# Kernel optimization log

Measured on AMD Instinct MI355X. Metric: run time of the kernel, lower is better.

## Reference

```python
import jax, jax.numpy as jnp
import numpy as np

E_LAYERS, D_MODEL, D_STATE, D_CONV, DT_RANK, D_FF = 2, 512, 16, 2, 32, 2048
BATCH, SEQ = 16, 512


def layer_norm(x, w, b, eps=1e-5):
    m = x.mean(-1, keepdims=True)
    v = ((x - m) ** 2).mean(-1, keepdims=True)
    return (x - m) / jnp.sqrt(v + eps) * w + b


def mamba(x, in_w, conv_w, conv_b, xproj_w, dt_w, dt_b, A_log, D_skip, out_w):
    # x: [B, L, D]; expand=1 so d_inner == D
    Bsz, L, D = x.shape
    N = A_log.shape[-1]
    R = dt_w.shape[-1]
    xz = x @ in_w.T                      # [B, L, 2D]
    xi, z = jnp.split(xz, 2, axis=-1)
    # causal depthwise conv1d, kernel K
    K = conv_w.shape[-1]
    xp = jnp.pad(xi.transpose(0, 2, 1), ((0, 0), (0, 0), (K - 1, 0)))  # [B, D, L+K-1]
    xc = jax.lax.conv_general_dilated(
        xp, conv_w[:, None, :], (1,), 'VALID',
        dimension_numbers=('NCH', 'OIH', 'NCH'), feature_group_count=D)  # [B, D, L]
    xc = jax.nn.silu(xc.transpose(0, 2, 1) + conv_b)                     # [B, L, D]
    proj = xc @ xproj_w.T                                                # [B, L, R+2N]
    dt, Bm, Cm = jnp.split(proj, [R, R + N], axis=-1)
    dt = jax.nn.softplus(dt @ dt_w.T + dt_b)                             # [B, L, D]
    A = -jnp.exp(A_log)                                                  # [D, N]
    dA = jnp.exp(dt[..., None] * A)                                      # [B, L, D, N]
    dBu = dt[..., None] * Bm[:, :, None, :] * xc[..., None]              # [B, L, D, N]

    def step(h, inp):
        a, b = inp
        h = a * h + b
        return h, h

    _, hs = jax.lax.scan(step, jnp.zeros((Bsz, D, N), x.dtype),
                         (dA.transpose(1, 0, 2, 3), dBu.transpose(1, 0, 2, 3)))
    y = jnp.einsum('lbdn,bln->bld', hs, Cm) + D_skip * xc
    return (y * jax.nn.silu(z)) @ out_w.T


def reference(x, in_w, conv_w, conv_b, xproj_w, dt_w, dt_b, A_log, D_skip, out_w,
              ffn1_w, ffn1_b, ffn2_w, ffn2_b, n1_w, n1_b, n2_w, n2_b, fn_w, fn_b):
    E = in_w.shape[0]
    for e in range(E):
        fwd = mamba(x, in_w[e, 0], conv_w[e, 0], conv_b[e, 0], xproj_w[e, 0],
                    dt_w[e, 0], dt_b[e, 0], A_log[e, 0], D_skip[e, 0], out_w[e, 0])
        xr = jnp.flip(x, axis=1)
        rev = mamba(xr, in_w[e, 1], conv_w[e, 1], conv_b[e, 1], xproj_w[e, 1],
                    dt_w[e, 1], dt_b[e, 1], A_log[e, 1], D_skip[e, 1], out_w[e, 1])
        x = x + fwd + jnp.flip(rev, axis=1)
        x = layer_norm(x, n1_w[e], n1_b[e])
        y = jax.nn.gelu(x @ ffn1_w[e].T + ffn1_b[e], approximate=False)
        y = y @ ffn2_w[e].T + ffn2_b[e]
        x = layer_norm(x + y, n2_w[e], n2_b[e])
    return layer_norm(x, fn_w, fn_b)


def setup_inputs() -> dict:
    key = jax.random.key(0)
    E, D, N, K, R, F = E_LAYERS, D_MODEL, D_STATE, D_CONV, DT_RANK, D_FF
    B, L = BATCH, SEQ
    ks = jax.random.split(key, 12)

    def rn(k, shape, s=0.02):
        return jax.random.normal(k, shape, jnp.float32) * s

    A_log = jnp.tile(jnp.log(jnp.arange(1, N + 1, dtype=jnp.float32)), (E, 2, D, 1))
    return {
        'x': jax.random.normal(ks[0], (B, L, D), jnp.float32),
        'in_w': rn(ks[1], (E, 2, 2 * D, D)),
        'conv_w': rn(ks[2], (E, 2, D, K), 0.5),
        'conv_b': jnp.zeros((E, 2, D), jnp.float32),
        'xproj_w': rn(ks[3], (E, 2, R + 2 * N, D)),
        'dt_w': rn(ks[4], (E, 2, D, R), 0.1),
        'dt_b': rn(ks[5], (E, 2, D), 0.1),
        'A_log': A_log,
        'D_skip': jnp.ones((E, 2, D), jnp.float32),
        'out_w': rn(ks[6], (E, 2, D, D)),
        'ffn1_w': rn(ks[7], (E, F, D)),
        'ffn1_b': jnp.zeros((E, F), jnp.float32),
        'ffn2_w': rn(ks[8], (E, D, F)),
        'ffn2_b': jnp.zeros((E, D), jnp.float32),
        'n1_w': jnp.ones((E, D), jnp.float32),
        'n1_b': jnp.zeros((E, D), jnp.float32),
        'n2_w': jnp.ones((E, D), jnp.float32),
        'n2_b': jnp.zeros((E, D), jnp.float32),
        'fn_w': jnp.ones((D,), jnp.float32),
        'fn_b': jnp.zeros((D,), jnp.float32),
    }
```

## Files before the change

### kernel.cpp

```cpp
#include <hip/hip_runtime.h>

#define BB 16
#define LL 512
#define DD 512
#define ROWS (BB*LL)

typedef unsigned short u16;
typedef __attribute__((ext_vector_type(8))) short short8;
typedef __attribute__((ext_vector_type(4))) float f32x4;
typedef __attribute__((ext_vector_type(4))) unsigned short u16x4;

__device__ __forceinline__ float b2f(u16 u) {
    return __uint_as_float(((unsigned int)u) << 16);
}
__device__ __forceinline__ u16 f2b(float f) {
    unsigned int u = __float_as_uint(f);
    u += 0x7FFFu + ((u >> 16) & 1u);
    return (u16)(u >> 16);
}
__device__ __forceinline__ float ld1(const void* p, size_t i, int f32) {
    return f32 ? ((const float*)p)[i] : b2f(((const u16*)p)[i]);
}
__device__ __forceinline__ float bf_elem(uint4 v, int j) {
    unsigned w = ((const unsigned*)&v)[j >> 1];
    return __uint_as_float((j & 1) ? (w & 0xFFFF0000u) : (w << 16));
}
__device__ __forceinline__ float red16(float x) {
    int v = __float_as_int(x);
    x += __int_as_float(__builtin_amdgcn_update_dpp(0, v, 0xB1, 0xF, 0xF, true));
    v = __float_as_int(x);
    x += __int_as_float(__builtin_amdgcn_update_dpp(0, v, 0x4E, 0xF, 0xF, true));
    v = __float_as_int(x);
    x += __int_as_float(__builtin_amdgcn_update_dpp(0, v, 0x141, 0xF, 0xF, true));
    v = __float_as_int(x);
    x += __int_as_float(__builtin_amdgcn_update_dpp(0, v, 0x140, 0xF, 0xF, true));
    return x;
}
__device__ __forceinline__ void gld16(const u16* g, u16* l) {
    __builtin_amdgcn_global_load_lds(
        (const __attribute__((address_space(1))) unsigned int*)g,
        (__attribute__((address_space(3))) unsigned int*)l, 16, 0, 0);
}

__global__ void detect(const u16* __restrict__ x, int* __restrict__ flag)
{
    __shared__ int s;
    if (threadIdx.x == 0) s = 0;
    __syncthreads();
    u16 v = x[2 * threadIdx.x] & 0x7FFFu;
    if ((v & 0x7F80u) >= 0x5000u) atomicOr(&s, 1);
    __syncthreads();
    if (threadIdx.x == 0) *flag = s;
}

__global__ __launch_bounds__(256)
void cvt_x(const void* __restrict__ X, float* __restrict__ acc, u16* __restrict__ cur,
           const int* __restrict__ flag)
{
    const int f = *flag;
    size_t i = (size_t)blockIdx.x * 256 + threadIdx.x;
    float v = ld1(X, i, f);
    acc[i] = v;
    cur[i] = f2b(v);
}

__global__ __launch_bounds__(256)
void cvt_copy(const void* __restrict__ src, u16* __restrict__ dst, int n,
              const int* __restrict__ flag)
{
    const int f = *flag;
    int i = blockIdx.x * 256 + threadIdx.x;
    if (i < n) dst[i] = f2b(ld1(src, i, f));
}

__global__ __launch_bounds__(256)
void cvt_xp2(const void* __restrict__ xp, u16* __restrict__ dst,
             const int* __restrict__ flag)
{
    const int f = *flag;
    int i = blockIdx.x * 256 + threadIdx.x;
    int e = i >> 17, r = (i >> 10) & 127, c = i & 1023;
    int dir = r >> 6, n = r & 63;
    float v = ((c >> 9) == dir)
        ? ld1(xp, ((size_t)(e*2 + dir)*64 + n)*512 + (c & 511), f) : 0.f;
    dst[i] = f2b(v);
}

__global__ __launch_bounds__(256)
void cvt_dt2(const void* __restrict__ dw, u16* __restrict__ dst,
             const int* __restrict__ flag)
{
    const int f = *flag;
    int i = blockIdx.x * 256 + threadIdx.x;
    int e = i >> 17, r = (i >> 7) & 1023, c = i & 127;
    int dir = r >> 9, d = r & 511;
    float v = 0.f;
    if (dir == 0 && c < 32)
        v = ld1(dw, ((size_t)(e*2)*512 + d)*32 + c, f);
    else if (dir == 1 && c >= 64 && c < 96)
        v = ld1(dw, ((size_t)(e*2 + 1)*512 + d)*32 + (c - 64), f);
    dst[i] = f2b(v);
}

__global__ __launch_bounds__(256)
void cvt_out2(const void* __restrict__ ow, u16* __restrict__ dst,
              const int* __restrict__ flag)
{
    const int f = *flag;
    int i = blockIdx.x * 256 + threadIdx.x;
    int e = i >> 19, rest = i & 524287;
    int d = rest >> 10, c = rest & 1023;
    int dir = c >> 9;
    dst[i] = f2b(ld1(ow, ((size_t)(e*2 + dir)*512 + d)*512 + (c & 511), f));
}

__global__ __launch_bounds__(256)
void acc_init(const u16* __restrict__ x, float* __restrict__ o)
{
    size_t i = (size_t)blockIdx.x * 256 + threadIdx.x;
    o[i] = b2f(x[i]);
}

__global__ __launch_bounds__(256)
void gemm_mfma(const u16* __restrict__ A, const u16* __restrict__ W,
               float* __restrict__ Cf, u16* __restrict__ Cb, u16* __restrict__ CbT,
               int M, int N, int K,
               const void* __restrict__ bias, size_t boff, int act, int accum,
               const int* __restrict__ flag)
{
    const int f = *flag;
    __shared__ u16 As[128][64];
    __shared__ u16 Ws[128][64];
    const int tid  = threadIdx.x;
    const int lane = tid & 63;
    const int wid  = tid >> 6;
    const int wr   = (wid >> 1) * 64;
    const int wc   = (wid & 1) * 64;
    const int row0 = blockIdx.y * 128;
    const int col0 = blockIdx.x * 128;
    const int mrow = lane & 15;
    const int kq   = (lane >> 4) * 8;
    const int swz  = (mrow & 7) << 3;
    const int kq0  = kq ^ swz;
    const int kq1  = (kq + 32) ^ swz;
    const int srow = wid * 32 + (lane >> 3);
    const int scol = (((lane & 7) ^ (lane >> 3)) & 7) * 8;
    const u16* gA = A + (size_t)(row0 + srow) * K + scol;
    const u16* gW = W + (size_t)(col0 + srow) * K + scol;
    u16* lA = &As[wid * 32][0];
    u16* lW = &Ws[wid * 32][0];

    f32x4 acc[4][4] = {};
    for (int k0 = 0; k0 < K; k0 += 64) {
        #pragma unroll
        for (int q = 0; q < 4; ++q) {
            gld16(gA + k0 + (size_t)(8 * q) * K, lA + 512 * q);
            gld16(gW + k0 + (size_t)(8 * q) * K, lW + 512 * q);
        }
        __syncthreads();
        #pragma unroll
        for (int kk = 0; kk < 2; ++kk) {
            const int kc = kk ? kq1 : kq0;
            short8 af[4], bfr[4];
            #pragma unroll
            for (int mi = 0; mi < 4; ++mi)
                af[mi] = *(const short8*)&As[wr + mi*16 + mrow][kc];
            #pragma unroll
            for (int ni = 0; ni < 4; ++ni)
                bfr[ni] = *(const short8*)&Ws[wc + ni*16 + mrow][kc];
            #pragma unroll
            for (int mi = 0; mi < 4; ++mi)
                #pragma unroll
                for (int ni = 0; ni < 4; ++ni)
                    acc[mi][ni] = __builtin_amdgcn_mfma_f32_16x16x32_bf16(
                        af[mi], bfr[ni], acc[mi][ni], 0, 0, 0);
        }
        __syncthreads();
    }
    const int drow = (lane >> 4) * 4;
    const int dcol = lane & 15;
    #pragma unroll
    for (int mi = 0; mi < 4; ++mi) {
        #pragma unroll
        for (int ni = 0; ni < 4; ++ni) {
            const int rowb = row0 + wr + mi*16 + drow;
            const int col  = col0 + wc + ni*16 + dcol;
            float bv = bias ? ld1(bias, boff + col, f) : 0.f;
            float vv[4];
            #pragma unroll
            for (int r = 0; r < 4; ++r) {
                float v = acc[mi][ni][r] + bv;
                if (act == 1) v = (v > 15.f) ? v : log1pf(__expf(v));
                else if (act == 2) v = 0.5f * v * (1.f + erff(v * 0.70710678118f));
                vv[r] = v;
            }
            if (accum) {
                #pragma unroll
                for (int r = 0; r < 4; ++r)
                    Cf[(size_t)(rowb + r) * N + col] += vv[r];
            } else if (Cf) {
                #pragma unroll
                for (int r = 0; r < 4; ++r)
                    Cf[(size_t)(rowb + r) * N + col] = vv[r];
            } else {
                if (Cb) {
                    #pragma unroll
                    for (int r = 0; r < 4; ++r)
                        Cb[(size_t)(rowb + r) * N + col] = f2b(vv[r]);
                }
                if (CbT) {
                    u16x4 pk;
                    #pragma unroll
                    for (int r = 0; r < 4; ++r) pk[r] = f2b(vv[r]);
                    *(u16x4*)(CbT + (size_t)col * M + rowb) = pk;
                }
            }
        }
    }
}

__global__ __launch_bounds__(256)
void conv_both(u16* __restrict__ xz, const void* __restrict__ cw,
               const void* __restrict__ cb, u16* __restrict__ xc, int e,
               const int* __restrict__ flag)
{
    const int f = *flag;
    int idx = blockIdx.x * 256 + threadIdx.x;
    int row = idx >> 10;
    int c = idx & 1023;
    int dir = c >> 9, d = c & 511;
    int l = row & (LL - 1);
    size_t base = (size_t)row * 2048 + dir * 1024;
    float xcur = b2f(xz[base + d]);
    int dsign = dir ? 1 : -1;
    int ln = l + dsign;
    float xnb = (ln >= 0 && ln < LL) ? b2f(xz[base + dsign*2048 + d]) : 0.f;
    size_t co = (size_t)(e*2 + dir) * 1024 + 2*d;
    float v = ld1(cw, co, f) * xnb + ld1(cw, co + 1, f) * xcur
            + ld1(cb, (size_t)(e*2 + dir)*512 + d, f);
    xc[(size_t)row * 1024 + c] = f2b(v / (1.f + __expf(-v)));
    float z = b2f(xz[base + 512 + d]);
    xz[base + 512 + d] = f2b(z / (1.f + __expf(-z)));
}

__global__ __launch_bounds__(256)
void transp(const u16* __restrict__ src, u16* __restrict__ dst)
{
    __shared__ u16 t[64][72];
    const int c0 = blockIdx.x * 64, r0 = blockIdx.y * 64;
    const int rr = threadIdx.x >> 3, cc = (threadIdx.x & 7) * 8;
    #pragma unroll
    for (int i = 0; i < 2; ++i) {
        uint4 v = *(const uint4*)(src + (size_t)(r0 + rr + i*32) * 1024 + c0 + cc);
        *(uint4*)&t[rr + i*32][cc] = v;
    }
    __syncthreads();
    const int tc = threadIdx.x >> 3, tr = (threadIdx.x & 7) * 8;
    #pragma unroll
    for (int i = 0; i < 2; ++i) {
        u16 tmp[8];
        #pragma unroll
        for (int j = 0; j < 8; ++j) tmp[j] = t[tr + j][tc + i*32];
        *(uint4*)(dst + (size_t)(c0 + tc + i*32) * 8192 + r0 + tr) = *(uint4*)tmp;
    }
}

template<int DIR>
__device__ __forceinline__ void scan_dir(
    const u16* __restrict__ dtp, const u16* __restrict__ xcp,
    const u16* __restrict__ Bp, const u16* __restrict__ Cp,
    const u16* __restrict__ zp, u16* __restrict__ gp,
    float Av, float Dv, int lane)
{
    float h = 0.f;
    int lb = DIR ? (LL - 8) : 0;
    const int stp = DIR ? -8 : 8;
    uint4 d8 = *(const uint4*)(dtp + lb);
    uint4 x8 = *(const uint4*)(xcp + lb);
    uint4 B8 = *(const uint4*)(Bp + lb);
    uint4 C8 = *(const uint4*)(Cp + lb);
    for (int it = 0; it < LL / 8; ++it) {
        const int lbn = lb + stp;
        uint4 nd = d8, nx = x8, nB = B8, nC = C8;
        if (it < LL / 8 - 1) {
            nd = *(const uint4*)(dtp + lbn);
            nx = *(const uint4*)(xcp + lbn);
            nB = *(const uint4*)(Bp + lbn);
            nC = *(const uint4*)(Cp + lbn);
        }
        float keep = 0.f;
        #pragma unroll
        for (int jj = 0; jj < 8; ++jj) {
            const int j = DIR ? (7 - jj) : jj;
            float dtv = bf_elem(d8, j);
            float xv  = bf_elem(x8, j);
            float Bn  = bf_elem(B8, j);
            float Cn  = bf_elem(C8, j);
            h = __expf(dtv * Av) * h + (dtv * xv) * Bn;
            float c = red16(h * Cn) + Dv * xv;
            keep = (lane == j) ? c : keep;
        }
        if (lane < 8) {
            float zs = b2f(zp[(lb + lane) * 2048]);
            gp[(lb + lane) * 1024] = f2b(keep * zs);
        }
        d8 = nd; x8 = nx; B8 = nB; C8 = nC;
        lb = lbn;
    }
}

__global__ __launch_bounds__(256)
void ssm_scan(u16* __restrict__ g, const u16* __restrict__ dtT,
              const u16* __restrict__ xcT, const u16* __restrict__ projT,
              const u16* __restrict__ xz,
              const void* __restrict__ A_log, const void* __restrict__ Dsk,
              int e, const int* __restrict__ flag)
{
    const int f = *flag;
    const int lane = threadIdx.x & 15;
    const int gg = blockIdx.x * 16 + (threadIdx.x >> 4);
    const int dir = gg >> 13;
    const int rem = gg & 8191;
    const int b = rem >> 9, d = rem & 511;
    const int ed = e * 2 + dir;
    const float Av = -__expf(ld1(A_log, (size_t)ed * 8192 + d * 16 + lane, f));
    const float Dv = ld1(Dsk, (size_t)ed * 512 + d, f);
    const int col = dir * 512 + d;
    const size_t tb = (size_t)col * 8192 + b * 512;
    const u16* dtp = dtT + tb;
    const u16* xcp = xcT + tb;
    const u16* Bp  = projT + (size_t)(dir * 64 + 32 + lane) * 8192 + b * 512;
    const u16* Cp  = Bp + (size_t)16 * 8192;
    u16* gp = g + (size_t)b * LL * 1024 + col;
    const u16* zp = xz + (size_t)b * LL * 2048 + dir * 1024 + 512 + d;
    if (dir == 0) scan_dir<0>(dtp, xcp, Bp, Cp, zp, gp, Av, Dv, lane);
    else          scan_dir<1>(dtp, xcp, Bp, Cp, zp, gp, Av, Dv, lane);
}

__global__ __launch_bounds__(256)
void lnorm(const u16* __restrict__ Xb, const float* __restrict__ Xf,
           const void* __restrict__ w, size_t wo, const void* __restrict__ b, size_t bo,
           void* __restrict__ out, int omode, const int* __restrict__ flag)
{
    const int f = *flag;
    int wid = (blockIdx.x * 256 + threadIdx.x) >> 6;
    int lane = threadIdx.x & 63;
    size_t base = (size_t)wid * DD;
    float v[8];
    float s = 0.f;
    #pragma unroll
    for (int i = 0; i < 8; ++i) {
        int c = lane + i*64;
        float t = 0.f;
        if (Xb) t += b2f(Xb[base + c]);
        if (Xf) t += Xf[base + c];
        v[i] = t; s += t;
    }
    #pragma unroll
    for (int off = 32; off > 0; off >>= 1) s += __shfl_xor(s, off);
    float mean = s * (1.f/512.f);
    float var = 0.f;
    #pragma unroll
    for (int i = 0; i < 8; ++i) { float dlt = v[i] - mean; var += dlt*dlt; }
    #pragma unroll
    for (int off = 32; off > 0; off >>= 1) var += __shfl_xor(var, off);
    float rstd = rsqrtf(var * (1.f/512.f) + 1e-5f);
    #pragma unroll
    for (int i = 0; i < 8; ++i) {
        int c = lane + i*64;
        float o = (v[i] - mean) * rstd * ld1(w, wo + c, f) + ld1(b, bo + c, f);
        if (omode && f) ((float*)out)[base + c] = o;
        else            ((u16*)out)[base + c] = f2b(o);
    }
}

extern "C" void kernel_launch(void* const* d_in, const int* in_sizes, int n_in,
                              void* d_out, int out_size, void* d_ws, size_t ws_size,
                              hipStream_t stream)
{
    (void)in_sizes; (void)n_in; (void)out_size; (void)ws_size;
    const void* X       = d_in[0];
    const void* in_w    = d_in[1];
    const void* conv_w  = d_in[2];
    const void* conv_b  = d_in[3];
    const void* xproj_w = d_in[4];
    const void* dt_w    = d_in[5];
    const void* dt_b    = d_in[6];
    const void* A_log   = d_in[7];
    const void* D_skip  = d_in[8];
    const void* out_w   = d_in[9];
    const void* ffn1_w  = d_in[10];
    const void* ffn1_b  = d_in[11];
    const void* ffn2_w  = d_in[12];
    const void* ffn2_b  = d_in[13];
    const void* n1_w    = d_in[14];
    const void* n1_b    = d_in[15];
    const void* n2_w    = d_in[16];
    const void* n2_b    = d_in[17];
    const void* fn_w    = d_in[18];
    const void* fn_b    = d_in[19];

    char* p = (char*)d_ws;
    float* acc   = (float*)(p);
    u16*   cur   = (u16*)(p + 16777216);
    u16*   xz    = (u16*)(p + 25165824);
    u16*   xc    = (u16*)(p + 58720256);
    u16*   dtT   = (u16*)(p + 58720256);
    u16*   g     = (u16*)(p + 75497472);
    u16*   proj  = (u16*)(p + 92274688);
    int*   flag  = (int*)(p + 94371840);
    u16*   wbf   = (u16*)(p + 94375936);
    u16*   xcT   = (u16*)(p + 110104576);
    u16*   projT = (u16*)(p + 126881792);
    u16*   ffh   = xz;
    float* y2    = (float*)xc;
    u16*   x1    = g;
    const size_t W_IN  = 0;
    const size_t W_XP  = 2097152;
    const size_t W_DT  = 2359296;
    const size_t W_OUT = 2621440;
    const size_t W_FF1 = 3670016;
    const size_t W_FF2 = 5767168;

    detect<<<1, 512, 0, stream>>>((const u16*)X, flag);
    cvt_x<<<ROWS*DD/256, 256, 0, stream>>>(X, acc, cur, flag);
    cvt_copy<<<2097152/256, 256, 0, stream>>>(in_w,   wbf + W_IN,  2097152, flag);
    cvt_copy<<<2097152/256, 256, 0, stream>>>(ffn1_w, wbf + W_FF1, 2097152, flag);
    cvt_copy<<<2097152/256, 256, 0, stream>>>(ffn2_w, wbf + W_FF2, 2097152, flag);
    cvt_xp2<<<262144/256, 256, 0, stream>>>(xproj_w, wbf + W_XP, flag);
    cvt_dt2<<<262144/256, 256, 0, stream>>>(dt_w, wbf + W_DT, flag);
    cvt_out2<<<1048576/256, 256, 0, stream>>>(out_w, wbf + W_OUT, flag);

    for (int e = 0; e < 2; ++e) {
        size_t eo = (size_t)e * 512;
        if (e == 1)
            acc_init<<<ROWS*DD/256, 256, 0, stream>>>(cur, acc);
        gemm_mfma<<<dim3(16,64), 256, 0, stream>>>(
            cur, wbf + W_IN + (size_t)e*1048576, nullptr, xz, nullptr,
            ROWS, 2048, 512, nullptr, 0, 0, 0, flag);
        conv_both<<<ROWS*1024/256, 256, 0, stream>>>(xz, conv_w, conv_b, xc, e, flag);
        transp<<<dim3(16,128), 256, 0, stream>>>(xc, xcT);
        gemm_mfma<<<dim3(1,64), 256, 0, stream>>>(
            xc, wbf + W_XP + (size_t)e*131072, nullptr, proj, projT,
            ROWS, 128, 1024, nullptr, 0, 0, 0, flag);
        gemm_mfma<<<dim3(8,64), 256, 0, stream>>>(
            proj, wbf + W_DT + (size_t)e*131072, nullptr, nullptr, dtT,
            ROWS, 1024, 128, dt_b, (size_t)e*1024, 1, 0, flag);
        ssm_scan<<<1024, 256, 0, stream>>>(g, dtT, xcT, projT, xz,
                                           A_log, D_skip, e, flag);
        gemm_mfma<<<dim3(4,64), 256, 0, stream>>>(
            g, wbf + W_OUT + (size_t)e*524288, acc, nullptr, nullptr,
            ROWS, 512, 1024, nullptr, 0, 0, 1, flag);
        lnorm<<<2048, 256, 0, stream>>>(nullptr, acc, n1_w, eo, n1_b, eo, x1, 0, flag);
        gemm_mfma<<<dim3(16,64), 256, 0, stream>>>(
            x1, wbf + W_FF1 + (size_t)e*1048576, nullptr, ffh, nullptr,
            ROWS, 2048, 512, ffn1_b, (size_t)e*2048, 2, 0, flag);
        gemm_mfma<<<dim3(4,64), 256, 0, stream>>>(
            ffh, wbf + W_FF2 + (size_t)e*1048576, y2, nullptr, nullptr,
            ROWS, 512, 2048, ffn2_b, eo, 0, 0, flag);
        lnorm<<<2048, 256, 0, stream>>>(x1, y2, n2_w, eo, n2_b, eo, cur, 0, flag);
    }
    lnorm<<<2048, 256, 0, stream>>>(cur, nullptr, fn_w, 0, fn_b, 0, d_out, 1, flag);
}
```

Before: 1.099 ms.

## Split-K the x_proj GEMM and fuse the weight-conversion and acc_init launches

The x_proj GEMM previously ran on only 64 workgroups. It now splits K four ways (grid z = 4), writing fp32 partial sums into scratch that reuses the g buffer. A new ksum kernel adds the partials into bf16 proj, and a separate transpose builds projT. The seven input and weight conversion kernels are merged into one cvt_all launch. acc_init is removed by having the layer-0 second layernorm also write its fp32 output into acc. This trades extra scratch traffic and two more small kernels for better GPU fill and fewer launches.

```diff
diff --git a/kernel.cpp b/kernel.cpp
--- a/kernel.cpp
+++ b/kernel.cpp
@@ -4,6 +4,13 @@
 #define LL 512
 #define DD 512
 #define ROWS (BB*LL)
+
+#define W_IN  0
+#define W_XP  2097152
+#define W_DT  2359296
+#define W_OUT 2621440
+#define W_FF1 3670016
+#define W_FF2 5767168
 
 typedef unsigned short u16;
 typedef __attribute__((ext_vector_type(8))) short short8;
@@ -54,71 +61,64 @@
 }
 
 __global__ __launch_bounds__(256)
-void cvt_x(const void* __restrict__ X, float* __restrict__ acc, u16* __restrict__ cur,
-           const int* __restrict__ flag)
+void cvt_all(const void* __restrict__ X, float* __restrict__ acc, u16* __restrict__ cur,
+             const void* __restrict__ in_w, const void* __restrict__ f1w,
+             const void* __restrict__ f2w, const void* __restrict__ xp,
+             const void* __restrict__ dw, const void* __restrict__ ow,
+             u16* __restrict__ wbf, const int* __restrict__ flag)
 {
     const int f = *flag;
-    size_t i = (size_t)blockIdx.x * 256 + threadIdx.x;
-    float v = ld1(X, i, f);
-    acc[i] = v;
-    cur[i] = f2b(v);
-}
-
-__global__ __launch_bounds__(256)
-void cvt_copy(const void* __restrict__ src, u16* __restrict__ dst, int n,
-              const int* __restrict__ flag)
-{
-    const int f = *flag;
+    size_t t = (size_t)blockIdx.x * 256 + threadIdx.x;
+    if (t < 4194304) {
+        float v = ld1(X, t, f);
+        acc[t] = v; cur[t] = f2b(v);
+        return;
+    }
+    t -= 4194304;
+    if (t < 2097152) { wbf[W_IN  + t] = f2b(ld1(in_w, t, f)); return; }
+    t -= 2097152;
+    if (t < 2097152) { wbf[W_FF1 + t] = f2b(ld1(f1w, t, f)); return; }
+    t -= 2097152;
+    if (t < 2097152) { wbf[W_FF2 + t] = f2b(ld1(f2w, t, f)); return; }
+    t -= 2097152;
+    if (t < 262144) {
+        int i = (int)t;
+        int e = i >> 17, r = (i >> 10) & 127, c = i & 1023;
+        int dir = r >> 6, n = r & 63;
+        float v = ((c >> 9) == dir)
+            ? ld1(xp, ((size_t)(e*2 + dir)*64 + n)*512 + (c & 511), f) : 0.f;
+        wbf[W_XP + i] = f2b(v);
+        return;
+    }
+    t -= 262144;
+    if (t < 262144) {
+        int i = (int)t;
+        int e = i >> 17, r = (i >> 7) & 1023, c = i & 127;
+        int dir = r >> 9, d = r & 511;
+        float v = 0.f;
+        if (dir == 0 && c < 32)
+            v = ld1(dw, ((size_t)(e*2)*512 + d)*32 + c, f);
+        else if (dir == 1 && c >= 64 && c < 96)
+            v = ld1(dw, ((size_t)(e*2 + 1)*512 + d)*32 + (c - 64), f);
+        wbf[W_DT + i] = f2b(v);
+        return;
+    }
+    t -= 262144;
+    {
+        int i = (int)t;
+        int e = i >> 19, rest = i & 524287;
+        int d = rest >> 10, c = rest & 1023;
+        int dir = c >> 9;
+        wbf[W_OUT + i] = f2b(ld1(ow, ((size_t)(e*2 + dir)*512 + d)*512 + (c & 511), f));
+    }
+}
+
+__global__ __launch_bounds__(256)
+void ksum(const float* __restrict__ psum, u16* __restrict__ proj)
+{
     int i = blockIdx.x * 256 + threadIdx.x;
-    if (i < n) dst[i] = f2b(ld1(src, i, f));
-}
-
-__global__ __launch_bounds__(256)
-void cvt_xp2(const void* __restrict__ xp, u16* __restrict__ dst,
-             const int* __restrict__ flag)
-{
-    const int f = *flag;
-    int i = blockIdx.x * 256 + threadIdx.x;
-    int e = i >> 17, r = (i >> 10) & 127, c = i & 1023;
-    int dir = r >> 6, n = r & 63;
-    float v = ((c >> 9) == dir)
-        ? ld1(xp, ((size_t)(e*2 + dir)*64 + n)*512 + (c & 511), f) : 0.f;
-    dst[i] = f2b(v);
-}
-
-__global__ __launch_bounds__(256)
-void cvt_dt2(const void* __restrict__ dw, u16* __restrict__ dst,
-             const int* __restrict__ flag)
-{
-    const int f = *flag;
-    int i = blockIdx.x * 256 + threadIdx.x;
-    int e = i >> 17, r = (i >> 7) & 1023, c = i & 127;
-    int dir = r >> 9, d = r & 511;
-    float v = 0.f;
-    if (dir == 0 && c < 32)
-        v = ld1(dw, ((size_t)(e*2)*512 + d)*32 + c, f);
-    else if (dir == 1 && c >= 64 && c < 96)
-        v = ld1(dw, ((size_t)(e*2 + 1)*512 + d)*32 + (c - 64), f);
-    dst[i] = f2b(v);
-}
-
-__global__ __launch_bounds__(256)
-void cvt_out2(const void* __restrict__ ow, u16* __restrict__ dst,
-              const int* __restrict__ flag)
-{
-    const int f = *flag;
-    int i = blockIdx.x * 256 + threadIdx.x;
-    int e = i >> 19, rest = i & 524287;
-    int d = rest >> 10, c = rest & 1023;
-    int dir = c >> 9;
-    dst[i] = f2b(ld1(ow, ((size_t)(e*2 + dir)*512 + d)*512 + (c & 511), f));
-}
-
-__global__ __launch_bounds__(256)
-void acc_init(const u16* __restrict__ x, float* __restrict__ o)
-{
-    size_t i = (size_t)blockIdx.x * 256 + threadIdx.x;
-    o[i] = b2f(x[i]);
+    float s = psum[i] + psum[i + 1048576] + psum[i + 2097152] + psum[i + 3145728];
+    proj[i] = f2b(s);
 }
 
 __global__ __launch_bounds__(256)
@@ -126,7 +126,7 @@
                float* __restrict__ Cf, u16* __restrict__ Cb, u16* __restrict__ CbT,
                int M, int N, int K,
                const void* __restrict__ bias, size_t boff, int act, int accum,
-               const int* __restrict__ flag)
+               int kcnt, const int* __restrict__ flag)
 {
     const int f = *flag;
     __shared__ u16 As[128][64];
@@ -149,9 +149,11 @@
     const u16* gW = W + (size_t)(col0 + srow) * K + scol;
     u16* lA = &As[wid * 32][0];
     u16* lW = &Ws[wid * 32][0];
+    const int kn = K / kcnt;
+    const int kb = blockIdx.z * kn;
 
     f32x4 acc[4][4] = {};
-    for (int k0 = 0; k0 < K; k0 += 64) {
+    for (int k0 = kb; k0 < kb + kn; k0 += 64) {
         #pragma unroll
         for (int q = 0; q < 4; ++q) {
             gld16(gA + k0 + (size_t)(8 * q) * K, lA + 512 * q);
@@ -177,6 +179,8 @@
         }
         __syncthreads();
     }
+    float* Cfz = Cf;
+    if (kcnt > 1) Cfz = Cf + (size_t)blockIdx.z * ((size_t)M * N);
     const int drow = (lane >> 4) * 4;
     const int dcol = lane & 15;
     #pragma unroll
@@ -201,7 +205,7 @@
             } else if (Cf) {
                 #pragma unroll
                 for (int r = 0; r < 4; ++r)
-                    Cf[(size_t)(rowb + r) * N + col] = vv[r];
+                    Cfz[(size_t)(rowb + r) * N + col] = vv[r];
             } else {
                 if (Cb) {
                     #pragma unroll
@@ -244,14 +248,14 @@
 }
 
 __global__ __launch_bounds__(256)
-void transp(const u16* __restrict__ src, u16* __restrict__ dst)
+void transp(const u16* __restrict__ src, u16* __restrict__ dst, int C)
 {
     __shared__ u16 t[64][72];
     const int c0 = blockIdx.x * 64, r0 = blockIdx.y * 64;
     const int rr = threadIdx.x >> 3, cc = (threadIdx.x & 7) * 8;
     #pragma unroll
     for (int i = 0; i < 2; ++i) {
-        uint4 v = *(const uint4*)(src + (size_t)(r0 + rr + i*32) * 1024 + c0 + cc);
+        uint4 v = *(const uint4*)(src + (size_t)(r0 + rr + i*32) * C + c0 + cc);
         *(uint4*)&t[rr + i*32][cc] = v;
     }
     __syncthreads();
@@ -340,7 +344,8 @@
 __global__ __launch_bounds__(256)
 void lnorm(const u16* __restrict__ Xb, const float* __restrict__ Xf,
            const void* __restrict__ w, size_t wo, const void* __restrict__ b, size_t bo,
-           void* __restrict__ out, int omode, const int* __restrict__ flag)
+           void* __restrict__ out, int omode, float* __restrict__ accf,
+           const int* __restrict__ flag)
 {
     const int f = *flag;
     int wid = (blockIdx.x * 256 + threadIdx.x) >> 6;
@@ -371,6 +376,7 @@
         float o = (v[i] - mean) * rstd * ld1(w, wo + c, f) + ld1(b, bo + c, f);
         if (omode && f) ((float*)out)[base + c] = o;
         else            ((u16*)out)[base + c] = f2b(o);
+        if (accf) accf[base + c] = o;
     }
 }
 
@@ -415,50 +421,43 @@
     u16*   ffh   = xz;
     float* y2    = (float*)xc;
     u16*   x1    = g;
-    const size_t W_IN  = 0;
-    const size_t W_XP  = 2097152;
-    const size_t W_DT  = 2359296;
-    const size_t W_OUT = 2621440;
-    const size_t W_FF1 = 3670016;
-    const size_t W_FF2 = 5767168;
+    float* psum  = (float*)g;
 
     detect<<<1, 512, 0, stream>>>((const u16*)X, flag);
-    cvt_x<<<ROWS*DD/256, 256, 0, stream>>>(X, acc, cur, flag);
-    cvt_copy<<<2097152/256, 256, 0, stream>>>(in_w,   wbf + W_IN,  2097152, flag);
-    cvt_copy<<<2097152/256, 256, 0, stream>>>(ffn1_w, wbf + W_FF1, 2097152, flag);
-    cvt_copy<<<2097152/256, 256, 0, stream>>>(ffn2_w, wbf + W_FF2, 2097152, flag);
-    cvt_xp2<<<262144/256, 256, 0, stream>>>(xproj_w, wbf + W_XP, flag);
-    cvt_dt2<<<262144/256, 256, 0, stream>>>(dt_w, wbf + W_DT, flag);
-    cvt_out2<<<1048576/256, 256, 0, stream>>>(out_w, wbf + W_OUT, flag);
+    cvt_all<<<47104, 256, 0, stream>>>(X, acc, cur, in_w, ffn1_w, ffn2_w,
+                                       xproj_w, dt_w, out_w, wbf, flag);
 
     for (int e = 0; e < 2; ++e) {
         size_t eo = (size_t)e * 512;
-        if (e == 1)
-            acc_init<<<ROWS*DD/256, 256, 0, stream>>>(cur, acc);
         gemm_mfma<<<dim3(16,64), 256, 0, stream>>>(
             cur, wbf + W_IN + (size_t)e*1048576, nullptr, xz, nullptr,
-            ROWS, 2048, 512, nullptr, 0, 0, 0, flag);
+            ROWS, 2048, 512, nullptr, 0, 0, 0, 1, flag);
         conv_both<<<ROWS*1024/256, 256, 0, stream>>>(xz, conv_w, conv_b, xc, e, flag);
-        transp<<<dim3(16,128), 256, 0, stream>>>(xc, xcT);
-        gemm_mfma<<<dim3(1,64), 256, 0, stream>>>(
-            xc, wbf + W_XP + (size_t)e*131072, nullptr, proj, projT,
-            ROWS, 128, 1024, nullptr, 0, 0, 0, flag);
+        transp<<<dim3(16,128), 256, 0, stream>>>(xc, xcT, 1024);
+        gemm_mfma<<<dim3(1,64,4), 256, 0, stream>>>(
+            xc, wbf + W_XP + (size_t)e*131072, psum, nullptr, nullptr,
+            ROWS, 128, 1024, nullptr, 0, 0, 0, 4, flag);
+        ksum<<<4096, 256, 0, stream>>>(psum, proj);
+        transp<<<dim3(2,128), 256, 0, stream>>>(proj, projT, 128);
         gemm_mfma<<<dim3(8,64), 256, 0, stream>>>(
             proj, wbf + W_DT + (size_t)e*131072, nullptr, nullptr, dtT,
-            ROWS, 1024, 128, dt_b, (size_t)e*1024, 1, 0, flag);
+            ROWS, 1024, 128, dt_b, (size_t)e*1024, 1, 0, 1, flag);
         ssm_scan<<<1024, 256, 0, stream>>>(g, dtT, xcT, projT, xz,
                                            A_log, D_skip, e, flag);
         gemm_mfma<<<dim3(4,64), 256, 0, stream>>>(
             g, wbf + W_OUT + (size_t)e*524288, acc, nullptr, nullptr,
-            ROWS, 512, 1024, nullptr, 0, 0, 1, flag);
-        lnorm<<<2048, 256, 0, stream>>>(nullptr, acc, n1_w, eo, n1_b, eo, x1, 0, flag);
+            ROWS, 512, 1024, nullptr, 0, 0, 1, 1, flag);
+        lnorm<<<2048, 256, 0, stream>>>(nullptr, acc, n1_w, eo, n1_b, eo, x1, 0,
+                                        nullptr, flag);
         gemm_mfma<<<dim3(16,64), 256, 0, stream>>>(
             x1, wbf + W_FF1 + (size_t)e*1048576, nullptr, ffh, nullptr,
-            ROWS, 2048, 512, ffn1_b, (size_t)e*2048, 2, 0, flag);
+            ROWS, 2048, 512, ffn1_b, (size_t)e*2048, 2, 0, 1, flag);
         gemm_mfma<<<dim3(4,64), 256, 0, stream>>>(
             ffh, wbf + W_FF2 + (size_t)e*1048576, y2, nullptr, nullptr,
-            ROWS, 512, 2048, ffn2_b, eo, 0, 0, flag);
-        lnorm<<<2048, 256, 0, stream>>>(x1, y2, n2_w, eo, n2_b, eo, cur, 0, flag);
-    }
-    lnorm<<<2048, 256, 0, stream>>>(cur, nullptr, fn_w, 0, fn_b, 0, d_out, 1, flag);
-}
+            ROWS, 512, 2048, ffn2_b, eo, 0, 0, 1, flag);
+        lnorm<<<2048, 256, 0, stream>>>(x1, y2, n2_w, eo, n2_b, eo, cur, 0,
+                                        (e == 0) ? acc : nullptr, flag);
+    }
+    lnorm<<<2048, 256, 0, stream>>>(cur, nullptr, fn_w, 0, fn_b, 0, d_out, 1,
+                                    nullptr, flag);
+}
```

Result: no change. 1.096 ms (-0.3%).
